# Performance work log

Measured on AMD Instinct MI355X. Metric: run time of the kernel, lower is better.

The kernel has to match this reference:

```python
import jax, jax.numpy as jnp
import numpy as np

MODES1 = 32
MODES2 = 32


def _dct1_last(x):
    # Unnormalized DCT-I along last axis via rfft of even-symmetric extension.
    # For length N input, extension [x0..x_{N-1}, x_{N-2}..x_1] has length 2(N-1);
    # rfft yields N real coefficients == scipy.fftpack.dct(x, type=1).
    ext = jnp.concatenate([x, x[..., -2:0:-1]], axis=-1)
    return jnp.fft.rfft(ext, axis=-1).real.astype(x.dtype)


def _dct1_2d(x):
    # DCT-I along last two axes (separable). scipy idct type-1 (unnormalized)
    # is identical to dct type-1, so this serves as both dctn and idctn.
    x = _dct1_last(x)
    x = jnp.swapaxes(x, -1, -2)
    x = _dct1_last(x)
    return jnp.swapaxes(x, -1, -2)


def setup_inputs() -> dict:
    key = jax.random.key(0)
    k1, k2, k3 = jax.random.split(key, 3)
    B, Cin, Cout, H, W = 8, 64, 64, 256, 256
    scale = 1.0 / (Cin * Cout)
    x = jax.random.normal(k1, (B, Cin, H, W), dtype=jnp.float32)
    weights1 = scale * jax.random.uniform(k2, (Cin, Cout, MODES1, MODES2), dtype=jnp.float32)
    weights2 = scale * jax.random.uniform(k3, (Cin, Cout, MODES1, MODES2), dtype=jnp.float32)
    return {"x": x, "weights1": weights1, "weights2": weights2}


def reference(x, weights1, weights2):
    B, Cin, H, W = x.shape
    Cout = weights1.shape[1]
    Wh = W // 2 + 1  # width of truncated spectral tensor (torch used cfloat, imag==0)
    m1, m2 = MODES1, MODES2

    x_dct = _dct1_2d(x)  # [B, Cin, H, W]

    low = jnp.einsum('bixy,ioxy->boxy', x_dct[:, :, :m1, :m2], weights1)
    high = jnp.einsum('bixy,ioxy->boxy', x_dct[:, :, -m1:, :m2], weights2)

    out_ft = jnp.zeros((B, Cout, H, Wh), dtype=x.dtype)
    out_ft = out_ft.at[:, :, :m1, :m2].set(low)
    out_ft = out_ft.at[:, :, H - m1:, :m2].set(high)

    # idctn(..., type=1, shape=(H, W)) zero-pads the last axis from Wh to W,
    # then applies unnormalized IDCT-I == DCT-I along axes 2,3.
    out_full = jnp.pad(out_ft, ((0, 0), (0, 0), (0, 0), (0, W - Wh)))
    return _dct1_2d(out_full)
```

## Files before the change

### kernel.cpp

```cpp
#include <hip/hip_runtime.h>
#include <math.h>

#define OFF_AT  0
#define OFF_BMT 16384
#define OFF_CMT 24576
#define OFF_DMT 40960
#define OFF_Y   49152
#define OFF_Z   1097728

__device__ __forceinline__ float cosT(int p) {
    int r = p % 510;
    if (r > 255) r = 510 - r;
    return cosf((float)r * (3.14159265358979323846f / 255.0f));
}

__global__ __launch_bounds__(256) void init_basis(float* __restrict__ ws) {
    int idx = blockIdx.x * 256 + threadIdx.x;
    if (idx < 16384) {
        int h = idx >> 6, r = idx & 63;
        int k1 = (r < 32) ? r : r + 192;
        float we = (h == 0 || h == 255) ? 1.f : 2.f;
        ws[OFF_AT + idx] = we * cosT(k1 * h);
    } else if (idx < 24576) {
        int j = idx - 16384; int w = j >> 5, y = j & 31;
        float we = (w == 0 || w == 255) ? 1.f : 2.f;
        ws[OFF_BMT + j] = we * cosT(y * w);
    } else if (idx < 40960) {
        int j = idx - 24576; int r = j >> 8, h = j & 255;
        int k1 = (r < 32) ? r : r + 192;
        float wsl = (r == 0 || r == 63) ? 1.f : 2.f;
        ws[OFF_CMT + j] = wsl * cosT(k1 * h);
    } else if (idx < 49152) {
        int j = idx - 40960; int y = j >> 8, w = j & 255;
        float wy = (y == 0) ? 1.f : 2.f;
        ws[OFF_DMT + j] = wy * cosT(y * w);
    }
}

__global__ __launch_bounds__(512, 4) void fwd_kernel(const float* __restrict__ x,
                                                     const float* __restrict__ ws,
                                                     float* __restrict__ Y) {
    __shared__ float lds[9216];
    const int t = threadIdx.x;
    const int bi = blockIdx.x;
    const float* xp = x + (size_t)bi * 65536;

    const int srow = t >> 2;
    const int scol = (t & 3) * 4;
    const int scolz = scol ^ (4 * ((srow >> 1) & 3));

    const int hb = t & 127;
    const int y8 = (t >> 7) * 8;
    const int csw = 4 * ((hb >> 1) & 3);

    float acc[2][8];
#pragma unroll
    for (int j = 0; j < 2; ++j)
#pragma unroll
        for (int yy = 0; yy < 8; ++yy) acc[j][yy] = 0.f;

    float4 sx0 = *(const float4*)(xp + srow * 256 + scol);
    float4 sx1 = *(const float4*)(xp + (srow + 128) * 256 + scol);
    float  sb  = ws[OFF_BMT + t];
    *(float4*)&lds[srow * 16 + scolz] = sx0;
    *(float4*)&lds[(srow + 128) * 16 + scolz] = sx1;
    lds[8192 + t] = sb;
    __syncthreads();

    for (int c = 0; c < 16; ++c) {
        const int cur = c & 1;
        if (c < 15) {
            const int wofs = (c + 1) * 16;
            sx0 = *(const float4*)(xp + srow * 256 + wofs + scol);
            sx1 = *(const float4*)(xp + (srow + 128) * 256 + wofs + scol);
            sb  = ws[OFF_BMT + (c + 1) * 512 + t];
        }
        const float* xs = lds + cur * 4096;
        const float* bs = lds + 8192 + cur * 512;
#pragma unroll
        for (int w = 0; w < 16; w += 4) {
            const int wz = w ^ csw;
            float4 xa = *(const float4*)&xs[hb * 16 + wz];
            float4 xc = *(const float4*)&xs[(hb + 128) * 16 + wz];
            const float xav[4] = {xa.x, xa.y, xa.z, xa.w};
            const float xcv[4] = {xc.x, xc.y, xc.z, xc.w};
#pragma unroll
            for (int k = 0; k < 4; ++k) {
                float4 b0 = *(const float4*)&bs[(w + k) * 32 + y8];
                float4 b1 = *(const float4*)&bs[(w + k) * 32 + y8 + 4];
                const float bv[8] = {b0.x, b0.y, b0.z, b0.w, b1.x, b1.y, b1.z, b1.w};
#pragma unroll
                for (int yy = 0; yy < 8; ++yy) {
                    acc[0][yy] += xav[k] * bv[yy];
                    acc[1][yy] += xcv[k] * bv[yy];
                }
            }
        }
        if (c < 15) {
            const int nxt = cur ^ 1;
            *(float4*)&lds[nxt * 4096 + srow * 16 + scolz] = sx0;
            *(float4*)&lds[nxt * 4096 + (srow + 128) * 16 + scolz] = sx1;
            lds[8192 + nxt * 512 + t] = sb;
        }
        __syncthreads();
    }

#pragma unroll
    for (int j = 0; j < 2; ++j) {
        const int row = hb + 128 * j;
        *(float4*)&lds[row * 36 + y8]     = make_float4(acc[j][0], acc[j][1], acc[j][2], acc[j][3]);
        *(float4*)&lds[row * 36 + y8 + 4] = make_float4(acc[j][4], acc[j][5], acc[j][6], acc[j][7]);
    }
    __syncthreads();

    const int r2 = t & 63;
    const int y4 = (t >> 6) * 4;
    float a2[4] = {0.f, 0.f, 0.f, 0.f};
    const float* At = ws + OFF_AT;
#pragma unroll 4
    for (int h = 0; h < 256; ++h) {
        const float av = At[h * 64 + r2];
        const float4 tv = *(const float4*)&lds[h * 36 + y4];
        a2[0] += av * tv.x; a2[1] += av * tv.y; a2[2] += av * tv.z; a2[3] += av * tv.w;
    }
    float* Yp = Y + (size_t)bi * 2048 + r2 * 32 + y4;
    *(float4*)Yp = make_float4(a2[0], a2[1], a2[2], a2[3]);
}

__global__ __launch_bounds__(256) void mix_kernel(const float* __restrict__ w1,
                                                  const float* __restrict__ w2,
                                                  const float* __restrict__ Yv,
                                                  float* __restrict__ Z) {
    const int r  = blockIdx.x & 63;
    const int og = blockIdx.x >> 6;
    const int t  = threadIdx.x;
    const int y  = (t & 15) * 2;
    const int o  = og * 4 + ((t >> 4) & 3);
    const int bp = t >> 6;

    const float* Wb = ((r < 32) ? (w1 + r * 32) : (w2 + (r - 32) * 32)) + o * 1024 + y;
    const float* Y0 = Yv + (size_t)(bp * 64) * 2048 + r * 32 + y;
    const float* Y1 = Y0 + (size_t)4 * 64 * 2048;

    float a00 = 0.f, a01 = 0.f, a10 = 0.f, a11 = 0.f;
#pragma unroll 4
    for (int i = 0; i < 64; ++i) {
        const float2 wv = *(const float2*)(Wb + (size_t)i * 65536);
        const float2 p  = *(const float2*)(Y0 + i * 2048);
        const float2 q  = *(const float2*)(Y1 + i * 2048);
        a00 += p.x * wv.x; a01 += p.y * wv.y;
        a10 += q.x * wv.x; a11 += q.y * wv.y;
    }
    float2 r0; r0.x = a00; r0.y = a01;
    float2 r1; r1.x = a10; r1.y = a11;
    *(float2*)(Z + (size_t)(bp * 64 + o) * 2048 + r * 32 + y) = r0;
    *(float2*)(Z + (size_t)((bp + 4) * 64 + o) * 2048 + r * 32 + y) = r1;
}

__global__ __launch_bounds__(512, 4) void inv_kernel(const float* __restrict__ ws,
                                                     const float* __restrict__ Zv,
                                                     float* __restrict__ out) {
    __shared__ float zs[2048];
    __shared__ float dmts[8192];
    __shared__ float t2t[4224];
    const int t = threadIdx.x;
    const int bo = blockIdx.x;
    const float* Zp = Zv + (size_t)bo * 2048;
    float* op = out + (size_t)bo * 65536;

    *(float4*)&zs[t * 4] = *(const float4*)(Zp + t * 4);
#pragma unroll
    for (int k = 0; k < 4; ++k)
        *(float4*)&dmts[k * 2048 + t * 4] = *(const float4*)(ws + OFF_DMT + k * 2048 + t * 4);
    __syncthreads();

    const int hb = t & 63;
    const int y4 = (t >> 6) * 4;
    const int wl = t & 31;
    const int hg = t >> 5;
    const int w0 = wl * 8;

    for (int hh = 0; hh < 2; ++hh) {
        float a1[2][4];
#pragma unroll
        for (int j = 0; j < 2; ++j)
#pragma unroll
            for (int k = 0; k < 4; ++k) a1[j][k] = 0.f;
        const float* Cm = ws + OFF_CMT + hh * 128 + hb;
#pragma unroll 2
        for (int r = 0; r < 64; ++r) {
            const float4 zv = *(const float4*)&zs[r * 32 + y4];
            const float av0 = Cm[r * 256];
            const float av1 = Cm[r * 256 + 64];
            a1[0][0] += av0 * zv.x; a1[0][1] += av0 * zv.y; a1[0][2] += av0 * zv.z; a1[0][3] += av0 * zv.w;
            a1[1][0] += av1 * zv.x; a1[1][1] += av1 * zv.y; a1[1][2] += av1 * zv.z; a1[1][3] += av1 * zv.w;
        }
#pragma unroll
        for (int j = 0; j < 2; ++j)
#pragma unroll
            for (int k = 0; k < 4; ++k)
                t2t[(y4 + k) * 132 + hb + 64 * j] = a1[j][k];
        __syncthreads();

        const int hbl = hg * 8;
        float a2[8][8];
#pragma unroll
        for (int ii = 0; ii < 8; ++ii)
#pragma unroll
            for (int ww = 0; ww < 8; ++ww) a2[ii][ww] = 0.f;
#pragma unroll 4
        for (int y = 0; y < 32; ++y) {
            const float4 ta = *(const float4*)&t2t[y * 132 + hbl];
            const float4 tb = *(const float4*)&t2t[y * 132 + hbl + 4];
            const float4 da = *(const float4*)&dmts[y * 256 + w0];
            const float4 db = *(const float4*)&dmts[y * 256 + w0 + 4];
            const float tv[8] = {ta.x, ta.y, ta.z, ta.w, tb.x, tb.y, tb.z, tb.w};
            const float dv[8] = {da.x, da.y, da.z, da.w, db.x, db.y, db.z, db.w};
#pragma unroll
            for (int ii = 0; ii < 8; ++ii)
#pragma unroll
                for (int ww = 0; ww < 8; ++ww)
                    a2[ii][ww] += tv[ii] * dv[ww];
        }
#pragma unroll
        for (int ii = 0; ii < 8; ++ii) {
            const int h = hh * 128 + hbl + ii;
            float* o8 = op + h * 256 + w0;
            *(float4*)o8       = make_float4(a2[ii][0], a2[ii][1], a2[ii][2], a2[ii][3]);
            *(float4*)(o8 + 4) = make_float4(a2[ii][4], a2[ii][5], a2[ii][6], a2[ii][7]);
        }
        __syncthreads();
    }
}

extern "C" void kernel_launch(void* const* d_in, const int* in_sizes, int n_in,
                              void* d_out, int out_size, void* d_ws, size_t ws_size,
                              hipStream_t stream) {
    const float* x  = (const float*)d_in[0];
    const float* w1 = (const float*)d_in[1];
    const float* w2 = (const float*)d_in[2];
    float* out = (float*)d_out;
    float* ws  = (float*)d_ws;

    hipLaunchKernelGGL(init_basis, dim3(192), dim3(256), 0, stream, ws);
    hipLaunchKernelGGL(fwd_kernel, dim3(512), dim3(512), 0, stream, x, ws, ws + OFF_Y);
    hipLaunchKernelGGL(mix_kernel, dim3(1024), dim3(256), 0, stream, w1, w2,
                       ws + OFF_Y, ws + OFF_Z);
    hipLaunchKernelGGL(inv_kernel, dim3(512), dim3(512), 0, stream, ws, ws + OFF_Z, out);
}
```

Baseline: 344.0 us.

## Exploit cosine even/odd symmetry to halve DCT matmul work in forward and inverse

```diff
diff --git a/kernel.cpp b/kernel.cpp
--- a/kernel.cpp
+++ b/kernel.cpp
@@ -1,12 +1,14 @@
 #include <hip/hip_runtime.h>
 #include <math.h>
 
-#define OFF_AT  0
-#define OFF_BMT 16384
-#define OFF_CMT 24576
-#define OFF_DMT 40960
-#define OFF_Y   49152
-#define OFF_Z   1097728
+#define OFF_BF 0
+#define OFF_AF 4096
+#define OFF_CF 12288
+#define OFF_DF 20480
+#define OFF_Y  24576
+#define OFF_Z  1073152
+
+#define F4E(v,k) ((k)==0?(v).x:(k)==1?(v).y:(k)==2?(v).z:(v).w)
 
 __device__ __forceinline__ float cosT(int p) {
     int r = p % 510;
@@ -16,115 +18,177 @@
 
 __global__ __launch_bounds__(256) void init_basis(float* __restrict__ ws) {
     int idx = blockIdx.x * 256 + threadIdx.x;
-    if (idx < 16384) {
-        int h = idx >> 6, r = idx & 63;
+    if (idx < 4096) {
+        int p = idx >> 11, w = (idx >> 4) & 127, yq = idx & 15;
+        ws[OFF_BF + idx] = cosT(w * (2 * yq + p));
+    } else if (idx < 12288) {
+        int j = idx - 4096; int h = j >> 6, r = j & 63;
         int k1 = (r < 32) ? r : r + 192;
-        float we = (h == 0 || h == 255) ? 1.f : 2.f;
-        ws[OFF_AT + idx] = we * cosT(k1 * h);
+        ws[OFF_AF + j] = cosT(k1 * h);
+    } else if (idx < 20480) {
+        int j = idx - 12288; int r = j >> 7, h = j & 127;
+        int k1 = (r < 32) ? r : r + 192;
+        float wr = (r == 0 || r == 63) ? 1.f : 2.f;
+        ws[OFF_CF + j] = wr * cosT(k1 * h);
     } else if (idx < 24576) {
-        int j = idx - 16384; int w = j >> 5, y = j & 31;
-        float we = (w == 0 || w == 255) ? 1.f : 2.f;
-        ws[OFF_BMT + j] = we * cosT(y * w);
-    } else if (idx < 40960) {
-        int j = idx - 24576; int r = j >> 8, h = j & 255;
-        int k1 = (r < 32) ? r : r + 192;
-        float wsl = (r == 0 || r == 63) ? 1.f : 2.f;
-        ws[OFF_CMT + j] = wsl * cosT(k1 * h);
-    } else if (idx < 49152) {
-        int j = idx - 40960; int y = j >> 8, w = j & 255;
+        int j = idx - 20480; int yp = j >> 11, yq = (j >> 7) & 15, w = j & 127;
+        int y = 2 * yq + yp;
         float wy = (y == 0) ? 1.f : 2.f;
-        ws[OFF_DMT + j] = wy * cosT(y * w);
-    }
-}
-
-__global__ __launch_bounds__(512, 4) void fwd_kernel(const float* __restrict__ x,
+        ws[OFF_DF + j] = wy * cosT(y * w);
+    }
+}
+
+__global__ __launch_bounds__(128, 1) void fwd_kernel(const float* __restrict__ x,
                                                      const float* __restrict__ ws,
                                                      float* __restrict__ Y) {
-    __shared__ float lds[9216];
+    __shared__ float lds[8192];
     const int t = threadIdx.x;
     const int bi = blockIdx.x;
     const float* xp = x + (size_t)bi * 65536;
 
-    const int srow = t >> 2;
-    const int scol = (t & 3) * 4;
-    const int scolz = scol ^ (4 * ((srow >> 1) & 3));
-
-    const int hb = t & 127;
-    const int y8 = (t >> 7) * 8;
-    const int csw = 4 * ((hb >> 1) & 3);
-
-    float acc[2][8];
-#pragma unroll
-    for (int j = 0; j < 2; ++j)
-#pragma unroll
-        for (int yy = 0; yy < 8; ++yy) acc[j][yy] = 0.f;
-
-    float4 sx0 = *(const float4*)(xp + srow * 256 + scol);
-    float4 sx1 = *(const float4*)(xp + (srow + 128) * 256 + scol);
-    float  sb  = ws[OFF_BMT + t];
-    *(float4*)&lds[srow * 16 + scolz] = sx0;
-    *(float4*)&lds[(srow + 128) * 16 + scolz] = sx1;
-    lds[8192 + t] = sb;
+#pragma unroll
+    for (int k = 0; k < 8; ++k) {
+        int i4 = k * 512 + t * 4;
+        *(float4*)&lds[4096 + i4] = *(const float4*)(ws + OFF_BF + i4);
+    }
+
+    const int sj = t & 1;
+    const int sj4 = 4 * sj;
+    const int r4 = t >> 1;
+
+    const int hb = t & 31;
+    const int yh = (t >> 5) & 1;
+    const int p  = t >> 6;
+    const int yb = yh * 8;
+
+    const int rows[8] = {hb, 127 - hb, 128 + hb, 255 - hb,
+                         hb + 32, 95 - hb, 160 + hb, 223 - hb};
+
+    float4 f0, f1, f2, f3, g0, g1, g2, g3;
+
+#define FWD_LOAD(cc) { \
+    int fb = 8 * (cc) + sj4, rb = 252 - 8 * (cc) - sj4; \
+    f0 = *(const float4*)(xp + (r4      ) * 256 + fb); \
+    f1 = *(const float4*)(xp + (r4 + 64 ) * 256 + fb); \
+    f2 = *(const float4*)(xp + (r4 + 128) * 256 + fb); \
+    f3 = *(const float4*)(xp + (r4 + 192) * 256 + fb); \
+    g0 = *(const float4*)(xp + (r4      ) * 256 + rb); \
+    g1 = *(const float4*)(xp + (r4 + 64 ) * 256 + rb); \
+    g2 = *(const float4*)(xp + (r4 + 128) * 256 + rb); \
+    g3 = *(const float4*)(xp + (r4 + 192) * 256 + rb); }
+
+#define FWD_STORE1(cc, FF, GG, M) { \
+    int rw = r4 + 64 * (M); \
+    int ps = rw * 8 + ((sj ^ ((rw >> 2) & 1)) << 2); \
+    float wA = ((cc) == 0 && sj == 0) ? 1.f : 2.f; \
+    float4 sp, sm; \
+    sp.x = wA  * (FF.x + GG.w); sm.x = wA  * (FF.x - GG.w); \
+    sp.y = 2.f * (FF.y + GG.z); sm.y = 2.f * (FF.y - GG.z); \
+    sp.z = 2.f * (FF.z + GG.y); sm.z = 2.f * (FF.z - GG.y); \
+    sp.w = 2.f * (FF.w + GG.x); sm.w = 2.f * (FF.w - GG.x); \
+    *(float4*)&lds[ps] = sp; *(float4*)&lds[2048 + ps] = sm; }
+
+#define FWD_STORE(cc) { FWD_STORE1(cc, f0, g0, 0); FWD_STORE1(cc, f1, g1, 1); \
+                        FWD_STORE1(cc, f2, g2, 2); FWD_STORE1(cc, f3, g3, 3); }
+
+    float acc[8][8];
+#pragma unroll
+    for (int m = 0; m < 8; ++m)
+#pragma unroll
+        for (int yy = 0; yy < 8; ++yy) acc[m][yy] = 0.f;
+
+    FWD_LOAD(0);
+    FWD_STORE(0);
     __syncthreads();
 
     for (int c = 0; c < 16; ++c) {
-        const int cur = c & 1;
+        if (c < 15) FWD_LOAD(c + 1);
+#pragma unroll
+        for (int jj = 0; jj < 2; ++jj) {
+            float4 sv[8];
+#pragma unroll
+            for (int m = 0; m < 8; ++m) {
+                int rw = rows[m];
+                sv[m] = *(float4*)&lds[p * 2048 + rw * 8 + ((jj ^ ((rw >> 2) & 1)) << 2)];
+            }
+#pragma unroll
+            for (int k = 0; k < 4; ++k) {
+                int wi = 8 * c + 4 * jj + k;
+                float4 b0 = *(float4*)&lds[4096 + p * 2048 + wi * 16 + yb];
+                float4 b1 = *(float4*)&lds[4096 + p * 2048 + wi * 16 + yb + 4];
+                float bv[8] = {b0.x, b0.y, b0.z, b0.w, b1.x, b1.y, b1.z, b1.w};
+#pragma unroll
+                for (int m = 0; m < 8; ++m) {
+                    float s = F4E(sv[m], k);
+#pragma unroll
+                    for (int yy = 0; yy < 8; ++yy) acc[m][yy] += s * bv[yy];
+                }
+            }
+        }
+        __syncthreads();
         if (c < 15) {
-            const int wofs = (c + 1) * 16;
-            sx0 = *(const float4*)(xp + srow * 256 + wofs + scol);
-            sx1 = *(const float4*)(xp + (srow + 128) * 256 + wofs + scol);
-            sb  = ws[OFF_BMT + (c + 1) * 512 + t];
-        }
-        const float* xs = lds + cur * 4096;
-        const float* bs = lds + 8192 + cur * 512;
-#pragma unroll
-        for (int w = 0; w < 16; w += 4) {
-            const int wz = w ^ csw;
-            float4 xa = *(const float4*)&xs[hb * 16 + wz];
-            float4 xc = *(const float4*)&xs[(hb + 128) * 16 + wz];
-            const float xav[4] = {xa.x, xa.y, xa.z, xa.w};
-            const float xcv[4] = {xc.x, xc.y, xc.z, xc.w};
+            FWD_STORE(c + 1);
+            __syncthreads();
+        }
+    }
+
+    {
+        const int s0 = 2 * yh, s1 = 2 * yh + 1;
+#define UWRITE(H, WGT, A, B) { \
+        int key = ((H) >> 1) & 3; \
+        float* up = &lds[p * 2048 + (H) * 16]; \
+        float* um = up + 4096; \
+        int p0 = (s0 ^ key) << 2, p1 = (s1 ^ key) << 2; \
+        *(float4*)&up[p0] = make_float4(WGT*(acc[A][0]+acc[B][0]), WGT*(acc[A][1]+acc[B][1]), \
+                                        WGT*(acc[A][2]+acc[B][2]), WGT*(acc[A][3]+acc[B][3])); \
+        *(float4*)&up[p1] = make_float4(WGT*(acc[A][4]+acc[B][4]), WGT*(acc[A][5]+acc[B][5]), \
+                                        WGT*(acc[A][6]+acc[B][6]), WGT*(acc[A][7]+acc[B][7])); \
+        *(float4*)&um[p0] = make_float4(WGT*(acc[A][0]-acc[B][0]), WGT*(acc[A][1]-acc[B][1]), \
+                                        WGT*(acc[A][2]-acc[B][2]), WGT*(acc[A][3]-acc[B][3])); \
+        *(float4*)&um[p1] = make_float4(WGT*(acc[A][4]-acc[B][4]), WGT*(acc[A][5]-acc[B][5]), \
+                                        WGT*(acc[A][6]-acc[B][6]), WGT*(acc[A][7]-acc[B][7])); }
+        float wq = (hb == 0) ? 1.f : 2.f;
+        UWRITE(hb,       wq,  0, 3);
+        UWRITE(127 - hb, 2.f, 1, 2);
+        UWRITE(hb + 32,  2.f, 4, 7);
+        UWRITE(95 - hb,  2.f, 5, 6);
+    }
+    __syncthreads();
+
+    {
+        const int par = t >> 6;
+        const int l = t & 63;
+        const int ys2 = l & 3;
+        const int idx4 = l >> 2;
+        const int rA = par + 4 * idx4, rB = rA + 2;
+        const float* Af = ws + OFF_AF;
+        float a2[2][2][4];
+#pragma unroll
+        for (int i = 0; i < 2; ++i)
+#pragma unroll
+            for (int j = 0; j < 2; ++j)
+#pragma unroll
+                for (int k = 0; k < 4; ++k) a2[i][j][k] = 0.f;
+#pragma unroll 4
+        for (int h = 0; h < 128; ++h) {
+            int sl = (ys2 ^ ((h >> 1) & 3)) << 2;
+            float4 u0 = *(float4*)&lds[par * 4096 + h * 16 + sl];
+            float4 u1 = *(float4*)&lds[par * 4096 + 2048 + h * 16 + sl];
+            float af0 = Af[h * 64 + rA];
+            float af1 = Af[h * 64 + rB];
 #pragma unroll
             for (int k = 0; k < 4; ++k) {
-                float4 b0 = *(const float4*)&bs[(w + k) * 32 + y8];
-                float4 b1 = *(const float4*)&bs[(w + k) * 32 + y8 + 4];
-                const float bv[8] = {b0.x, b0.y, b0.z, b0.w, b1.x, b1.y, b1.z, b1.w};
-#pragma unroll
-                for (int yy = 0; yy < 8; ++yy) {
-                    acc[0][yy] += xav[k] * bv[yy];
-                    acc[1][yy] += xcv[k] * bv[yy];
-                }
-            }
-        }
-        if (c < 15) {
-            const int nxt = cur ^ 1;
-            *(float4*)&lds[nxt * 4096 + srow * 16 + scolz] = sx0;
-            *(float4*)&lds[nxt * 4096 + (srow + 128) * 16 + scolz] = sx1;
-            lds[8192 + nxt * 512 + t] = sb;
-        }
-        __syncthreads();
-    }
-
-#pragma unroll
-    for (int j = 0; j < 2; ++j) {
-        const int row = hb + 128 * j;
-        *(float4*)&lds[row * 36 + y8]     = make_float4(acc[j][0], acc[j][1], acc[j][2], acc[j][3]);
-        *(float4*)&lds[row * 36 + y8 + 4] = make_float4(acc[j][4], acc[j][5], acc[j][6], acc[j][7]);
-    }
-    __syncthreads();
-
-    const int r2 = t & 63;
-    const int y4 = (t >> 6) * 4;
-    float a2[4] = {0.f, 0.f, 0.f, 0.f};
-    const float* At = ws + OFF_AT;
-#pragma unroll 4
-    for (int h = 0; h < 256; ++h) {
-        const float av = At[h * 64 + r2];
-        const float4 tv = *(const float4*)&lds[h * 36 + y4];
-        a2[0] += av * tv.x; a2[1] += av * tv.y; a2[2] += av * tv.z; a2[3] += av * tv.w;
-    }
-    float* Yp = Y + (size_t)bi * 2048 + r2 * 32 + y4;
-    *(float4*)Yp = make_float4(a2[0], a2[1], a2[2], a2[3]);
+                float e0 = F4E(u0, k), e1 = F4E(u1, k);
+                a2[0][0][k] += af0 * e0; a2[0][1][k] += af0 * e1;
+                a2[1][0][k] += af1 * e0; a2[1][1][k] += af1 * e1;
+            }
+        }
+        float* Yp = Y + (size_t)bi * 2048;
+        *(float4*)(Yp + rA * 32      + 4 * ys2) = make_float4(a2[0][0][0], a2[0][0][1], a2[0][0][2], a2[0][0][3]);
+        *(float4*)(Yp + rA * 32 + 16 + 4 * ys2) = make_float4(a2[0][1][0], a2[0][1][1], a2[0][1][2], a2[0][1][3]);
+        *(float4*)(Yp + rB * 32      + 4 * ys2) = make_float4(a2[1][0][0], a2[1][0][1], a2[1][0][2], a2[1][0][3]);
+        *(float4*)(Yp + rB * 32 + 16 + 4 * ys2) = make_float4(a2[1][1][0], a2[1][1][1], a2[1][1][2], a2[1][1][3]);
+    }
 }
 
 __global__ __launch_bounds__(256) void mix_kernel(const float* __restrict__ w1,
@@ -134,102 +198,153 @@
     const int r  = blockIdx.x & 63;
     const int og = blockIdx.x >> 6;
     const int t  = threadIdx.x;
-    const int y  = (t & 15) * 2;
+    const int ys = t & 15;
     const int o  = og * 4 + ((t >> 4) & 3);
     const int bp = t >> 6;
 
-    const float* Wb = ((r < 32) ? (w1 + r * 32) : (w2 + (r - 32) * 32)) + o * 1024 + y;
-    const float* Y0 = Yv + (size_t)(bp * 64) * 2048 + r * 32 + y;
+    const float* Wb = ((r < 32) ? (w1 + r * 32) : (w2 + (r - 32) * 32)) + o * 1024 + 2 * ys;
+    const float* Y0 = Yv + (size_t)(bp * 64) * 2048 + r * 32 + ys;
     const float* Y1 = Y0 + (size_t)4 * 64 * 2048;
 
     float a00 = 0.f, a01 = 0.f, a10 = 0.f, a11 = 0.f;
 #pragma unroll 4
     for (int i = 0; i < 64; ++i) {
-        const float2 wv = *(const float2*)(Wb + (size_t)i * 65536);
-        const float2 p  = *(const float2*)(Y0 + i * 2048);
-        const float2 q  = *(const float2*)(Y1 + i * 2048);
-        a00 += p.x * wv.x; a01 += p.y * wv.y;
-        a10 += q.x * wv.x; a11 += q.y * wv.y;
+        float2 wv = *(const float2*)(Wb + (size_t)i * 65536);
+        float pe = Y0[i * 2048], po = Y0[i * 2048 + 16];
+        float qe = Y1[i * 2048], qo = Y1[i * 2048 + 16];
+        a00 += pe * wv.x; a01 += po * wv.y;
+        a10 += qe * wv.x; a11 += qo * wv.y;
     }
     float2 r0; r0.x = a00; r0.y = a01;
     float2 r1; r1.x = a10; r1.y = a11;
-    *(float2*)(Z + (size_t)(bp * 64 + o) * 2048 + r * 32 + y) = r0;
-    *(float2*)(Z + (size_t)((bp + 4) * 64 + o) * 2048 + r * 32 + y) = r1;
-}
-
-__global__ __launch_bounds__(512, 4) void inv_kernel(const float* __restrict__ ws,
+    *(float2*)(Z + (size_t)(bp * 64 + o) * 2048 + r * 32 + 2 * ys) = r0;
+    *(float2*)(Z + (size_t)((bp + 4) * 64 + o) * 2048 + r * 32 + 2 * ys) = r1;
+}
+
+__global__ __launch_bounds__(256, 2) void inv_kernel(const float* __restrict__ ws,
                                                      const float* __restrict__ Zv,
                                                      float* __restrict__ out) {
-    __shared__ float zs[2048];
-    __shared__ float dmts[8192];
-    __shared__ float t2t[4224];
+    __shared__ float lds[14336];
     const int t = threadIdx.x;
-    const int bo = blockIdx.x;
-    const float* Zp = Zv + (size_t)bo * 2048;
-    float* op = out + (size_t)bo * 65536;
-
-    *(float4*)&zs[t * 4] = *(const float4*)(Zp + t * 4);
-#pragma unroll
-    for (int k = 0; k < 4; ++k)
-        *(float4*)&dmts[k * 2048 + t * 4] = *(const float4*)(ws + OFF_DMT + k * 2048 + t * 4);
+    const float* Zp = Zv + (size_t)blockIdx.x * 2048;
+    float* op = out + (size_t)blockIdx.x * 65536;
+
+#pragma unroll
+    for (int k = 0; k < 4; ++k) {
+        int i4 = k * 1024 + t * 4;
+        *(float4*)&lds[10240 + i4] = *(const float4*)(ws + OFF_DF + i4);
+    }
+    {
+        int base = t * 8;
+        int r = base >> 5;
+        int q = (base & 31) >> 1;
+        float4 v0 = *(const float4*)(Zp + base);
+        float4 v1 = *(const float4*)(Zp + base + 4);
+        float* z0 = &lds[r * 16];
+        float* z1 = &lds[1024 + r * 16];
+        z0[q]     = v0.x; z1[q]     = v0.y; z0[q + 1] = v0.z; z1[q + 1] = v0.w;
+        z0[q + 2] = v1.x; z1[q + 2] = v1.y; z0[q + 3] = v1.z; z1[q + 3] = v1.w;
+    }
     __syncthreads();
 
-    const int hb = t & 63;
-    const int y4 = (t >> 6) * 4;
-    const int wl = t & 31;
-    const int hg = t >> 5;
-    const int w0 = wl * 8;
-
-    for (int hh = 0; hh < 2; ++hh) {
-        float a1[2][4];
-#pragma unroll
-        for (int j = 0; j < 2; ++j)
-#pragma unroll
-            for (int k = 0; k < 4; ++k) a1[j][k] = 0.f;
-        const float* Cm = ws + OFF_CMT + hh * 128 + hb;
+    {
+        const int hb = t & 63;
+        const int q4 = t >> 6;
+        const int zp = q4 & 1;
+        const int yh = q4 >> 1;
+        const int yb = yh * 8;
+        float aE0[8], aE1[8], aO0[8], aO1[8];
+#pragma unroll
+        for (int k = 0; k < 8; ++k) { aE0[k] = aE1[k] = aO0[k] = aO1[k] = 0.f; }
+        const float* Cfp = ws + OFF_CF + hb;
 #pragma unroll 2
-        for (int r = 0; r < 64; ++r) {
-            const float4 zv = *(const float4*)&zs[r * 32 + y4];
-            const float av0 = Cm[r * 256];
-            const float av1 = Cm[r * 256 + 64];
-            a1[0][0] += av0 * zv.x; a1[0][1] += av0 * zv.y; a1[0][2] += av0 * zv.z; a1[0][3] += av0 * zv.w;
-            a1[1][0] += av1 * zv.x; a1[1][1] += av1 * zv.y; a1[1][2] += av1 * zv.z; a1[1][3] += av1 * zv.w;
-        }
-#pragma unroll
-        for (int j = 0; j < 2; ++j)
-#pragma unroll
-            for (int k = 0; k < 4; ++k)
-                t2t[(y4 + k) * 132 + hb + 64 * j] = a1[j][k];
-        __syncthreads();
-
-        const int hbl = hg * 8;
-        float a2[8][8];
-#pragma unroll
-        for (int ii = 0; ii < 8; ++ii)
-#pragma unroll
-            for (int ww = 0; ww < 8; ++ww) a2[ii][ww] = 0.f;
-#pragma unroll 4
-        for (int y = 0; y < 32; ++y) {
-            const float4 ta = *(const float4*)&t2t[y * 132 + hbl];
-            const float4 tb = *(const float4*)&t2t[y * 132 + hbl + 4];
-            const float4 da = *(const float4*)&dmts[y * 256 + w0];
-            const float4 db = *(const float4*)&dmts[y * 256 + w0 + 4];
-            const float tv[8] = {ta.x, ta.y, ta.z, ta.w, tb.x, tb.y, tb.z, tb.w};
-            const float dv[8] = {da.x, da.y, da.z, da.w, db.x, db.y, db.z, db.w};
-#pragma unroll
-            for (int ii = 0; ii < 8; ++ii)
-#pragma unroll
-                for (int ww = 0; ww < 8; ++ww)
-                    a2[ii][ww] += tv[ii] * dv[ww];
-        }
-#pragma unroll
-        for (int ii = 0; ii < 8; ++ii) {
-            const int h = hh * 128 + hbl + ii;
-            float* o8 = op + h * 256 + w0;
-            *(float4*)o8       = make_float4(a2[ii][0], a2[ii][1], a2[ii][2], a2[ii][3]);
-            *(float4*)(o8 + 4) = make_float4(a2[ii][4], a2[ii][5], a2[ii][6], a2[ii][7]);
-        }
-        __syncthreads();
+        for (int rr = 0; rr < 32; ++rr) {
+            int re = 2 * rr, ro = 2 * rr + 1;
+            float c0 = Cfp[re * 128], c1 = Cfp[re * 128 + 64];
+            float4 z0 = *(float4*)&lds[zp * 1024 + re * 16 + yb];
+            float4 z1 = *(float4*)&lds[zp * 1024 + re * 16 + yb + 4];
+            float zv[8] = {z0.x, z0.y, z0.z, z0.w, z1.x, z1.y, z1.z, z1.w};
+#pragma unroll
+            for (int k = 0; k < 8; ++k) { aE0[k] += c0 * zv[k]; aE1[k] += c1 * zv[k]; }
+            float c2 = Cfp[ro * 128], c3 = Cfp[ro * 128 + 64];
+            float4 z2 = *(float4*)&lds[zp * 1024 + ro * 16 + yb];
+            float4 z3 = *(float4*)&lds[zp * 1024 + ro * 16 + yb + 4];
+            float zw[8] = {z2.x, z2.y, z2.z, z2.w, z3.x, z3.y, z3.z, z3.w};
+#pragma unroll
+            for (int k = 0; k < 8; ++k) { aO0[k] += c2 * zw[k]; aO1[k] += c3 * zw[k]; }
+        }
+        const int s0 = 2 * yh, s1 = 2 * yh + 1;
+#define T2WRITE(H, A, B, SGN) { \
+        int key = ((H) >> 1) & 3; \
+        float* tp = &lds[2048 + zp * 4096 + (H) * 16]; \
+        *(float4*)&tp[(s0 ^ key) << 2] = make_float4(A[0] SGN B[0], A[1] SGN B[1], A[2] SGN B[2], A[3] SGN B[3]); \
+        *(float4*)&tp[(s1 ^ key) << 2] = make_float4(A[4] SGN B[4], A[5] SGN B[5], A[6] SGN B[6], A[7] SGN B[7]); }
+        T2WRITE(hb,       aE0, aO0, +);
+        T2WRITE(hb + 64,  aE1, aO1, +);
+        T2WRITE(255 - hb, aE0, aO0, -);
+        T2WRITE(191 - hb, aE1, aO1, -);
+    }
+    __syncthreads();
+
+    {
+        const int wg = t & 7;
+        const int hg2 = (t >> 3) & 31;
+        for (int hh = 0; hh < 2; ++hh) {
+            const int h0 = hg2 + 128 * hh;
+            float P[4][4][4], Q[4][4][4];
+#pragma unroll
+            for (int j = 0; j < 4; ++j)
+#pragma unroll
+                for (int m = 0; m < 4; ++m)
+#pragma unroll
+                    for (int e = 0; e < 4; ++e) { P[j][m][e] = 0.f; Q[j][m][e] = 0.f; }
+#pragma unroll
+            for (int yp = 0; yp < 2; ++yp) {
+#pragma unroll
+                for (int yg = 0; yg < 4; ++yg) {
+                    float4 tv[4];
+#pragma unroll
+                    for (int j = 0; j < 4; ++j) {
+                        int hj = h0 + 32 * j;
+                        tv[j] = *(float4*)&lds[2048 + yp * 4096 + hj * 16 + ((yg ^ ((hj >> 1) & 3)) << 2)];
+                    }
+#pragma unroll
+                    for (int k = 0; k < 4; ++k) {
+                        int yq = 4 * yg + k;
+                        float4 dv[4];
+#pragma unroll
+                        for (int m = 0; m < 4; ++m)
+                            dv[m] = *(float4*)&lds[10240 + yp * 2048 + yq * 128 + 4 * wg + 32 * m];
+#pragma unroll
+                        for (int j = 0; j < 4; ++j) {
+                            float tvv = F4E(tv[j], k);
+#pragma unroll
+                            for (int m = 0; m < 4; ++m)
+#pragma unroll
+                                for (int e = 0; e < 4; ++e) {
+                                    float pr = tvv * F4E(dv[m], e);
+                                    if (yp == 0) P[j][m][e] += pr; else Q[j][m][e] += pr;
+                                }
+                        }
+                    }
+                }
+            }
+#pragma unroll
+            for (int j = 0; j < 4; ++j) {
+                int h = h0 + 32 * j;
+                float* orow = op + h * 256;
+#pragma unroll
+                for (int m = 0; m < 4; ++m) {
+                    float4 fw, mv;
+                    fw.x = P[j][m][0] + Q[j][m][0]; fw.y = P[j][m][1] + Q[j][m][1];
+                    fw.z = P[j][m][2] + Q[j][m][2]; fw.w = P[j][m][3] + Q[j][m][3];
+                    mv.x = P[j][m][3] - Q[j][m][3]; mv.y = P[j][m][2] - Q[j][m][2];
+                    mv.z = P[j][m][1] - Q[j][m][1]; mv.w = P[j][m][0] - Q[j][m][0];
+                    *(float4*)(orow + 4 * wg + 32 * m) = fw;
+                    *(float4*)(orow + 252 - 4 * wg - 32 * m) = mv;
+                }
+            }
+        }
     }
 }
 
@@ -242,9 +357,9 @@
     float* out = (float*)d_out;
     float* ws  = (float*)d_ws;
 
-    hipLaunchKernelGGL(init_basis, dim3(192), dim3(256), 0, stream, ws);
-    hipLaunchKernelGGL(fwd_kernel, dim3(512), dim3(512), 0, stream, x, ws, ws + OFF_Y);
+    hipLaunchKernelGGL(init_basis, dim3(96), dim3(256), 0, stream, ws);
+    hipLaunchKernelGGL(fwd_kernel, dim3(512), dim3(128), 0, stream, x, ws, ws + OFF_Y);
     hipLaunchKernelGGL(mix_kernel, dim3(1024), dim3(256), 0, stream, w1, w2,
                        ws + OFF_Y, ws + OFF_Z);
-    hipLaunchKernelGGL(inv_kernel, dim3(512), dim3(512), 0, stream, ws, ws + OFF_Z, out);
-}
+    hipLaunchKernelGGL(inv_kernel, dim3(512), dim3(256), 0, stream, ws, ws + OFF_Z, out);
+}
```

Result: slower. 539.1 us (+56.7%).
